# Performance work log

Hardware: AMD Instinct MI355X
Metric: run time of the kernel (lower is better)

## Reference

```python
import jax, jax.numpy as jnp
import numpy as np

N = 100_000      # num nodes
E = 6_400_000    # num edges
P = 12           # periods
F = 32           # output_size (TGCN hidden)


def setup_inputs() -> dict:
    key = jax.random.key(0)
    ks = jax.random.split(key, 16)
    g = lambda i, shape, s=0.1: jax.random.normal(ks[i], shape, dtype=jnp.float32) * s
    zf = jnp.zeros((F,), jnp.float32)
    return {
        "x": jax.random.normal(ks[0], (N, P), dtype=jnp.float32),
        "edge_index": jax.random.randint(ks[1], (2, E), 0, N, dtype=jnp.int64),
        "edge_weight": jax.random.uniform(ks[2], (E,), dtype=jnp.float32),
        "attention": g(3, (P,), 1.0),            # A3TGCN learned period attention
        # GCNConv weights: in_channels=1 -> weight is effectively a length-F vector
        "wc_z": g(4, (F,)), "bc_z": zf,
        "wc_r": g(5, (F,)), "bc_r": zf,
        "wc_h": g(6, (F,)), "bc_h": zf,
        # TGCN gate linears: Linear(2F, F) with bias
        "wl_z": g(7, (2 * F, F)), "bl_z": zf,
        "wl_r": g(8, (2 * F, F)), "bl_r": zf,
        "wl_h": g(9, (2 * F, F)), "bl_h": zf,
        # final Linear(F, 1)
        "w_out": g(10, (F, 1)), "b_out": jnp.zeros((1,), jnp.float32),
    }


def reference(x, edge_index, edge_weight, attention,
              wc_z, bc_z, wc_r, bc_r, wc_h, bc_h,
              wl_z, bl_z, wl_r, bl_r, wl_h, bl_h,
              w_out, b_out):
    n = x.shape[0]
    src, dst = edge_index[0], edge_index[1]

    # GCN normalization with added self-loops (weight 1): D^{-1/2} (A + I) D^{-1/2}
    deg = jax.ops.segment_sum(edge_weight, dst, num_segments=n) + 1.0
    dinv = jax.lax.rsqrt(deg)
    norm = dinv[src] * edge_weight * dinv[dst]          # (E,)

    # GCNConv is linear and in_channels == 1, so conv_g(X_p)_i = agg(X_p)_i * W_g + b_g
    # where agg is the normalized (self-loop augmented) scalar aggregation.
    # Aggregate all periods at once: (E, P) messages -> (N, P)
    agg = jax.ops.segment_sum(norm[:, None] * x[src], dst, num_segments=n)
    agg = agg + (dinv * dinv)[:, None] * x              # self-loop term, (N, P)

    probs = jax.nn.softmax(attention)                   # (P,)
    H0 = jnp.zeros((n, F), x.dtype)                     # A3TGCN calls TGCN with H=None each period
    H_acc = jnp.zeros((n, F), x.dtype)
    for p in range(P):                                  # small fixed structural loop
        s = agg[:, p, None]                             # (N, 1)
        conv_z = s * wc_z + bc_z                        # (N, F)
        conv_r = s * wc_r + bc_r
        conv_h = s * wc_h + bc_h
        Z = jax.nn.sigmoid(jnp.concatenate([conv_z, H0], axis=1) @ wl_z + bl_z)
        R = jax.nn.sigmoid(jnp.concatenate([conv_r, H0], axis=1) @ wl_r + bl_r)
        Ht = jnp.tanh(jnp.concatenate([conv_h, H0 * R], axis=1) @ wl_h + bl_h)
        Hp = Z * H0 + (1.0 - Z) * Ht                    # TGCN single step from zero state
        H_acc = H_acc + probs[p] * Hp

    h = jax.nn.relu(H_acc)
    return h @ w_out + b_out                            # (N, 1)
```

## Files before the change

kernel.cpp:

```cpp
#include <hip/hip_runtime.h>

#define NN 100000
#define EE 6400000
#define PP 12
#define FF 32

#define VV   128
#define BB   782
#define CAP  8832
#define K1B  800
#define CHK  8000
#define NBIN 784
#define AST  13
#define XST  16
#define NR   18

__global__ void precompute_k(const float* __restrict__ att,
                             const float* __restrict__ wc_z, const float* __restrict__ bc_z,
                             const float* __restrict__ wc_h, const float* __restrict__ bc_h,
                             const float* __restrict__ wl_z, const float* __restrict__ bl_z,
                             const float* __restrict__ wl_h, const float* __restrict__ bl_h,
                             float* __restrict__ tabs) {
    int j = threadIdx.x;
    if (j < FF) {
        float az = 0.f, cz = 0.f, ah = 0.f, ch = 0.f;
        for (int f = 0; f < FF; ++f) {
            float wz = wl_z[f * FF + j];
            float wh = wl_h[f * FF + j];
            az += wc_z[f] * wz;
            cz += bc_z[f] * wz;
            ah += wc_h[f] * wh;
            ch += bc_h[f] * wh;
        }
        tabs[16 + j]          = az;
        tabs[16 + FF + j]     = cz + bl_z[j];
        tabs[16 + 2 * FF + j] = ah;
        tabs[16 + 3 * FF + j] = ch + bl_h[j];
    } else if (j == FF) {
        float a[PP];
        float m = -1e30f;
        for (int p = 0; p < PP; ++p) { a[p] = att[p]; m = fmaxf(m, a[p]); }
        float s = 0.f;
        for (int p = 0; p < PP; ++p) { a[p] = __expf(a[p] - m); s += a[p]; }
        for (int p = 0; p < PP; ++p) tabs[p] = a[p] / s;
    }
}

__global__ __launch_bounds__(512) void bucketsort_k(const int* __restrict__ src,
                                                    const int* __restrict__ dst,
                                                    const float* __restrict__ ew,
                                                    uint2* __restrict__ recs,
                                                    unsigned short* __restrict__ T16) {
    __shared__ unsigned int perm[CHK];
    __shared__ int hist[NBIN];
    __shared__ int offs[NBIN];
    int tid = threadIdx.x;
    int blk = blockIdx.x;
    int beg = blk * CHK;

    for (int b = tid; b < NBIN; b += 512) hist[b] = 0;
    __syncthreads();

    for (int e = tid; e < CHK; e += 512)
        atomicAdd(&hist[dst[beg + e] >> 7], 1);
    __syncthreads();

    int i2   = 512 + tid;
    int own0 = hist[tid];
    int own1 = (i2 < NBIN) ? hist[i2] : 0;
    for (int off = 1; off < NBIN; off <<= 1) {
        int a0 = (tid >= off) ? hist[tid - off] : 0;
        int a1 = (i2 < NBIN) ? hist[i2 - off] : 0;
        __syncthreads();
        hist[tid] += a0;
        if (i2 < NBIN) hist[i2] += a1;
        __syncthreads();
    }
    offs[tid] = hist[tid] - own0;
    if (i2 < NBIN) offs[i2] = hist[i2] - own1;
    __syncthreads();

    for (int b = tid; b < BB + 1; b += 512)
        T16[(size_t)b * K1B + blk] = (unsigned short)offs[b];
    __syncthreads();

    for (int e = tid; e < CHK; e += 512) {
        int d = dst[beg + e];
        int p = atomicAdd(&offs[d >> 7], 1);
        perm[p] = ((unsigned)(d & (VV - 1)) << 13) | (unsigned)e;
    }
    __syncthreads();

    uint2* o = recs + (size_t)blk * CHK;
    for (int k = tid; k < CHK; k += 512) {
        unsigned pe = perm[k];
        int e = (int)(pe & 0x1FFFu);
        uint2 r;
        r.x = ((pe >> 13) << 17) | (unsigned)src[beg + e];
        r.y = __float_as_uint(ew[beg + e]);
        o[k] = r;
    }
}

__global__ __launch_bounds__(512) void deg2_k(const uint2* __restrict__ recs,
                                              const unsigned short* __restrict__ T16,
                                              const float* __restrict__ x,
                                              float* __restrict__ xds) {
    __shared__ unsigned long long wsum[VV];
    __shared__ int rstart[K1B];
    __shared__ int rpre[K1B + 1];
    int b = blockIdx.x;
    int tid = threadIdx.x;
    int i1 = tid + 512;

    if (tid < VV) wsum[tid] = 0ull;
    for (int k = tid; k < K1B; k += 512) {
        int s = T16[(size_t)b * K1B + k];
        int e = T16[(size_t)(b + 1) * K1B + k];
        rstart[k] = s;
        rpre[k]   = e - s;
    }
    __syncthreads();

    for (int off = 1; off < K1B; off <<= 1) {
        int a0 = (tid >= off) ? rpre[tid - off] : 0;
        int a1 = (i1 < K1B) ? rpre[i1 - off] : 0;
        __syncthreads();
        rpre[tid] += a0;
        if (i1 < K1B) rpre[i1] += a1;
        __syncthreads();
    }
    int inc0 = rpre[tid];
    int inc1 = (i1 < K1B) ? rpre[i1] : 0;
    __syncthreads();
    if (tid == 0) rpre[0] = 0;
    rpre[tid + 1] = inc0;
    if (i1 < K1B) rpre[i1 + 1] = inc1;
    __syncthreads();

    int n = rpre[K1B];
    for (int k = tid; k < n; k += 512) {
        int r = 0;
        #pragma unroll
        for (int s = 512; s; s >>= 1) {
            int c = r + s;
            if (c < K1B && rpre[c] <= k) r = c;
        }
        uint2 v = recs[(size_t)r * CHK + rstart[r] + (k - rpre[r])];
        unsigned long long w = (unsigned long long)(__uint_as_float(v.y) * 4294967296.0f);
        atomicAdd(&wsum[v.x >> 17], w);
    }
    __syncthreads();

    int node = b * VV + tid;
    if (tid < VV && node < NN) {
        float wf = (float)wsum[tid] * (1.0f / 4294967296.0f);
        float dv = rsqrtf(wf + 1.0f);
        const float4* xr = (const float4*)(x + (size_t)node * PP);
        float4* xo = (float4*)(xds + ((size_t)node << 4));
        #pragma unroll
        for (int q = 0; q < 3; ++q) {
            float4 v = xr[q];
            v.x *= dv; v.y *= dv; v.z *= dv; v.w *= dv;
            xo[q] = v;
        }
        xds[((size_t)node << 4) + 12] = dv;
    }
}

__global__ __launch_bounds__(512) void sortagg_k(const uint2* __restrict__ recs,
                                                 const unsigned short* __restrict__ T16,
                                                 const float* __restrict__ xds,
                                                 const float* __restrict__ tabs,
                                                 const float* __restrict__ w_out,
                                                 const float* __restrict__ b_out,
                                                 float* __restrict__ out) {
    __shared__ uint2 srec[CAP];
    __shared__ int   h[VV], starts_s[VV], offs[VV], cnts_s[VV];
    __shared__ int   rstart[K1B];
    __shared__ int   rpre[K1B + 1];
    int b = blockIdx.x;
    int tid = threadIdx.x;
    int i1 = tid + 512;

    if (tid < VV) h[tid] = 0;
    for (int k = tid; k < K1B; k += 512) {
        int s = T16[(size_t)b * K1B + k];
        int e = T16[(size_t)(b + 1) * K1B + k];
        rstart[k] = s;
        rpre[k]   = e - s;
    }
    __syncthreads();

    for (int off = 1; off < K1B; off <<= 1) {
        int a0 = (tid >= off) ? rpre[tid - off] : 0;
        int a1 = (i1 < K1B) ? rpre[i1 - off] : 0;
        __syncthreads();
        rpre[tid] += a0;
        if (i1 < K1B) rpre[i1] += a1;
        __syncthreads();
    }
    int inc0 = rpre[tid];
    int inc1 = (i1 < K1B) ? rpre[i1] : 0;
    __syncthreads();
    if (tid == 0) rpre[0] = 0;
    rpre[tid + 1] = inc0;
    if (i1 < K1B) rpre[i1 + 1] = inc1;
    __syncthreads();

    int n = min(rpre[K1B], 512 * NR);

    uint2 regs[NR];
    #pragma unroll
    for (int w = 0; w < NR; ++w) {
        int k = tid + w * 512;
        if (k < n) {
            int r = 0;
            #pragma unroll
            for (int s = 512; s; s >>= 1) {
                int c = r + s;
                if (c < K1B && rpre[c] <= k) r = c;
            }
            uint2 v = recs[(size_t)r * CHK + rstart[r] + (k - rpre[r])];
            regs[w] = v;
            atomicAdd(&h[v.x >> 17], 1);
        }
    }
    __syncthreads();

    int own = (tid < VV) ? h[tid] : 0;
    #pragma unroll
    for (int off = 1; off < VV; off <<= 1) {
        int t = (tid < VV && tid >= off) ? h[tid - off] : 0;
        __syncthreads();
        if (tid < VV) h[tid] += t;
        __syncthreads();
    }
    if (tid < VV) {
        int pre = h[tid] - own;
        starts_s[tid] = pre;
        offs[tid]     = pre;
        cnts_s[tid]   = own;
    }
    __syncthreads();

    #pragma unroll
    for (int w = 0; w < NR; ++w) {
        int k = tid + w * 512;
        if (k < n) {
            uint2 v = regs[w];
            int p = atomicAdd(&offs[v.x >> 17], 1);
            if (p < CAP) srec[p] = v;
        }
    }
    __syncthreads();

    float acc[PP];
    {
        int local = tid >> 2;
        int q     = tid & 3;
        int st = min(starts_s[local], CAP);
        int en = min(starts_s[local] + cnts_s[local], CAP);
        int cn = en - st;

        #pragma unroll
        for (int p = 0; p < PP; ++p) acc[p] = 0.f;

        for (int m = q; m < cn; m += 4) {
            uint2 v = srec[st + m];
            float c = __uint_as_float(v.y);
            const float4* xs = (const float4*)(xds + ((size_t)(v.x & 0x1FFFFu) << 4));
            float4 v0 = xs[0], v1 = xs[1], v2 = xs[2];
            acc[0] += c * v0.x;  acc[1] += c * v0.y;  acc[2]  += c * v0.z;  acc[3]  += c * v0.w;
            acc[4] += c * v1.x;  acc[5] += c * v1.y;  acc[6]  += c * v1.z;  acc[7]  += c * v1.w;
            acc[8] += c * v2.x;  acc[9] += c * v2.y;  acc[10] += c * v2.z;  acc[11] += c * v2.w;
        }

        #pragma unroll
        for (int p = 0; p < PP; ++p) {
            acc[p] += __shfl_xor(acc[p], 1, 4);
            acc[p] += __shfl_xor(acc[p], 2, 4);
        }
    }
    __syncthreads();

    float* agg = (float*)srec;
    if ((tid & 3) == 0) {
        float* ap = &agg[(tid >> 2) * AST];
        #pragma unroll
        for (int p = 0; p < PP; ++p) ap[p] = acc[p];
    }
    __syncthreads();

    int g = tid >> 5;
    int j = tid & 31;
    float azj = tabs[16 + j];
    float czj = tabs[16 + FF + j];
    float ahj = tabs[16 + 2 * FF + j];
    float chj = tabs[16 + 3 * FF + j];

    for (int nl = g; nl < VV; nl += 16) {
        int i = b * VV + nl;
        if (i >= NN) continue;
        float dv = xds[((size_t)i << 4) + 12];
        const float* ai = &agg[nl * AST];

        float accum = 0.f;
        #pragma unroll
        for (int p = 0; p < PP; ++p) {
            float sp = dv * (ai[p] + xds[((size_t)i << 4) + p]);
            float pr = tabs[p];
            float uz = sp * azj + czj;
            float uh = sp * ahj + chj;
            float one_minus_z = 1.0f / (1.0f + __expf(uz));
            float e2h = __expf(2.0f * uh);
            float th  = 1.0f - 2.0f / (e2h + 1.0f);
            accum += pr * one_minus_z * th;
        }
        float hv = fmaxf(accum, 0.f) * w_out[j];
        #pragma unroll
        for (int off = 16; off > 0; off >>= 1)
            hv += __shfl_xor(hv, off, 32);
        if (j == 0) out[i] = hv + b_out[0];
    }
}

__global__ __launch_bounds__(256) void deg_k(const int* __restrict__ dst,
                                             const float* __restrict__ ew,
                                             float* __restrict__ deg) {
    int stride = gridDim.x * blockDim.x;
    for (int e = blockIdx.x * blockDim.x + threadIdx.x; e < EE; e += stride)
        atomicAdd(&deg[dst[e]], ew[e]);
}

__global__ __launch_bounds__(256) void dinv_self_k(const float* __restrict__ x,
                                                   float* __restrict__ deg,
                                                   float* __restrict__ agg) {
    int i = blockIdx.x * blockDim.x + threadIdx.x;
    if (i >= NN) return;
    float d  = deg[i] + 1.0f;
    float dv = rsqrtf(d);
    deg[i]   = dv;
    float dv2 = dv * dv;
    const float4* xr = (const float4*)(x + (size_t)i * PP);
    float4* ar = (float4*)(agg + (size_t)i * PP);
    #pragma unroll
    for (int q = 0; q < 3; ++q) {
        float4 v = xr[q];
        v.x *= dv2; v.y *= dv2; v.z *= dv2; v.w *= dv2;
        ar[q] = v;
    }
}

__global__ __launch_bounds__(256) void agg_k(const int* __restrict__ src,
                                             const int* __restrict__ dst,
                                             const float* __restrict__ ew,
                                             const float* __restrict__ x,
                                             const float* __restrict__ dinv,
                                             float* __restrict__ agg) {
    int stride = gridDim.x * blockDim.x;
    for (int e = blockIdx.x * blockDim.x + threadIdx.x; e < EE; e += stride) {
        int s = src[e];
        int d = dst[e];
        float nw = dinv[s] * ew[e] * dinv[d];
        const float4* xs = (const float4*)(x + (size_t)s * PP);
        float* ad = agg + (size_t)d * PP;
        float4 v0 = xs[0], v1 = xs[1], v2 = xs[2];
        atomicAdd(&ad[0],  nw * v0.x);
        atomicAdd(&ad[1],  nw * v0.y);
        atomicAdd(&ad[2],  nw * v0.z);
        atomicAdd(&ad[3],  nw * v0.w);
        atomicAdd(&ad[4],  nw * v1.x);
        atomicAdd(&ad[5],  nw * v1.y);
        atomicAdd(&ad[6],  nw * v1.z);
        atomicAdd(&ad[7],  nw * v1.w);
        atomicAdd(&ad[8],  nw * v2.x);
        atomicAdd(&ad[9],  nw * v2.y);
        atomicAdd(&ad[10], nw * v2.z);
        atomicAdd(&ad[11], nw * v2.w);
    }
}

__global__ __launch_bounds__(256) void node_k(const float* __restrict__ agg,
                                              const float* __restrict__ tabs,
                                              const float* __restrict__ w_out,
                                              const float* __restrict__ b_out,
                                              float* __restrict__ out) {
    int t = blockIdx.x * blockDim.x + threadIdx.x;
    int i = t >> 5;
    int j = t & 31;
    if (i >= NN) return;
    float azj = tabs[16 + j];
    float czj = tabs[16 + FF + j];
    float ahj = tabs[16 + 2 * FF + j];
    float chj = tabs[16 + 3 * FF + j];
    float acc = 0.f;
    #pragma unroll
    for (int p = 0; p < PP; ++p) {
        float s  = agg[i * PP + p];
        float pr = tabs[p];
        float uz = s * azj + czj;
        float uh = s * ahj + chj;
        float one_minus_z = 1.0f / (1.0f + __expf(uz));
        float e2h = __expf(2.0f * uh);
        float th  = 1.0f - 2.0f / (e2h + 1.0f);
        acc += pr * one_minus_z * th;
    }
    float h = fmaxf(acc, 0.f) * w_out[j];
    #pragma unroll
    for (int off = 16; off > 0; off >>= 1)
        h += __shfl_xor(h, off, 32);
    if (j == 0) out[i] = h + b_out[0];
}

extern "C" void kernel_launch(void* const* d_in, const int* in_sizes, int n_in,
                              void* d_out, int out_size, void* d_ws, size_t ws_size,
                              hipStream_t stream) {
    const float* x    = (const float*)d_in[0];
    const int*   ei   = (const int*)d_in[1];
    const float* ew   = (const float*)d_in[2];
    const float* att  = (const float*)d_in[3];
    const float* wc_z = (const float*)d_in[4];
    const float* bc_z = (const float*)d_in[5];
    const float* wc_h = (const float*)d_in[8];
    const float* bc_h = (const float*)d_in[9];
    const float* wl_z = (const float*)d_in[10];
    const float* bl_z = (const float*)d_in[11];
    const float* wl_h = (const float*)d_in[14];
    const float* bl_h = (const float*)d_in[15];
    const float* wout = (const float*)d_in[16];
    const float* bout = (const float*)d_in[17];
    float* out = (float*)d_out;

    const int* src = ei;
    const int* dst = ei + EE;

    size_t region = (size_t)EE * sizeof(uint2);
    size_t tbl_sz = (size_t)783 * K1B * sizeof(unsigned short);
    size_t xds_sz = (size_t)NN * XST * sizeof(float);
    size_t need   = region + tbl_sz + xds_sz + 4096;

    if (ws_size >= need) {
        uint2*          recs = (uint2*)d_ws;
        unsigned short* T16  = (unsigned short*)((char*)d_ws + region);
        float*          xds  = (float*)((char*)d_ws + region + tbl_sz);
        float*          tabs = (float*)((char*)d_ws + region + tbl_sz + xds_sz);

        precompute_k<<<1, 64, 0, stream>>>(att, wc_z, bc_z, wc_h, bc_h, wl_z, bl_z, wl_h, bl_h, tabs);
        bucketsort_k<<<K1B, 512, 0, stream>>>(src, dst, ew, recs, T16);
        deg2_k<<<BB, 512, 0, stream>>>(recs, T16, x, xds);
        sortagg_k<<<BB, 512, 0, stream>>>(recs, T16, xds, tabs, wout, bout, out);
    } else {
        float* deg  = (float*)d_ws;
        float* agg  = deg + NN;
        float* tabs = agg + (size_t)NN * PP;

        hipMemsetAsync(deg, 0, NN * sizeof(float), stream);
        precompute_k<<<1, 64, 0, stream>>>(att, wc_z, bc_z, wc_h, bc_h, wl_z, bl_z, wl_h, bl_h, tabs);
        deg_k<<<4096, 256, 0, stream>>>(dst, ew, deg);
        dinv_self_k<<<(NN + 255) / 256, 256, 0, stream>>>(x, deg, agg);
        agg_k<<<8192, 256, 0, stream>>>(src, dst, ew, x, deg, agg);
        node_k<<<NN * 32 / 256, 256, 0, stream>>>(agg, tabs, wout, bout, out);
    }
}
```

Before: 357.0 us.

## Split per-bucket degree and aggregation work across two segment blocks

The degree and aggregation kernels now launch two blocks per 128-node bucket, each handling half of the 800 sort chunks. Partial degree sums and partial aggregates go to global buffers, and new xds_k and epi_k kernels combine them. The intent is to raise parallelism and occupancy by halving shared memory and register records per block (CAP2, NR2). The cost is two extra kernel launches and extra global traffic for the partial results.

```diff
diff --git a/kernel.cpp b/kernel.cpp
--- a/kernel.cpp
+++ b/kernel.cpp
@@ -5,15 +5,16 @@
 #define PP 12
 #define FF 32
 
-#define VV   128
-#define BB   782
-#define CAP  8832
-#define K1B  800
-#define CHK  8000
-#define NBIN 784
-#define AST  13
-#define XST  16
-#define NR   18
+#define VV    128
+#define BB    782
+#define K1B   800
+#define CHK   8000
+#define NBIN  784
+#define XST   16
+#define K1SEG 400
+#define CAP2  4576
+#define NR2   9
+#define FPSI  (1.0f / 4294967296.0f)
 
 __global__ void precompute_k(const float* __restrict__ att,
                              const float* __restrict__ wc_z, const float* __restrict__ bc_z,
@@ -104,124 +105,121 @@
 
 __global__ __launch_bounds__(512) void deg2_k(const uint2* __restrict__ recs,
                                               const unsigned short* __restrict__ T16,
-                                              const float* __restrict__ x,
-                                              float* __restrict__ xds) {
+                                              unsigned long long* __restrict__ pdeg) {
     __shared__ unsigned long long wsum[VV];
-    __shared__ int rstart[K1B];
-    __shared__ int rpre[K1B + 1];
-    int b = blockIdx.x;
+    __shared__ unsigned short rstart[K1SEG];
+    __shared__ int rpre[K1SEG + 1];
+    int b   = blockIdx.x >> 1;
+    int seg = blockIdx.x & 1;
     int tid = threadIdx.x;
-    int i1 = tid + 512;
+    int k0  = seg * K1SEG;
 
     if (tid < VV) wsum[tid] = 0ull;
-    for (int k = tid; k < K1B; k += 512) {
-        int s = T16[(size_t)b * K1B + k];
-        int e = T16[(size_t)(b + 1) * K1B + k];
-        rstart[k] = s;
-        rpre[k]   = e - s;
-    }
-    __syncthreads();
-
-    for (int off = 1; off < K1B; off <<= 1) {
-        int a0 = (tid >= off) ? rpre[tid - off] : 0;
-        int a1 = (i1 < K1B) ? rpre[i1 - off] : 0;
-        __syncthreads();
-        rpre[tid] += a0;
-        if (i1 < K1B) rpre[i1] += a1;
-        __syncthreads();
-    }
-    int inc0 = rpre[tid];
-    int inc1 = (i1 < K1B) ? rpre[i1] : 0;
+    if (tid < K1SEG) {
+        int s = T16[(size_t)b * K1B + k0 + tid];
+        int e = T16[(size_t)(b + 1) * K1B + k0 + tid];
+        rstart[tid] = (unsigned short)s;
+        rpre[tid]   = e - s;
+    }
+    __syncthreads();
+
+    for (int off = 1; off < K1SEG; off <<= 1) {
+        int a = (tid < K1SEG && tid >= off) ? rpre[tid - off] : 0;
+        __syncthreads();
+        if (tid < K1SEG) rpre[tid] += a;
+        __syncthreads();
+    }
+    int inc = (tid < K1SEG) ? rpre[tid] : 0;
     __syncthreads();
     if (tid == 0) rpre[0] = 0;
-    rpre[tid + 1] = inc0;
-    if (i1 < K1B) rpre[i1 + 1] = inc1;
-    __syncthreads();
-
-    int n = rpre[K1B];
+    if (tid < K1SEG) rpre[tid + 1] = inc;
+    __syncthreads();
+
+    int n = rpre[K1SEG];
     for (int k = tid; k < n; k += 512) {
         int r = 0;
         #pragma unroll
-        for (int s = 512; s; s >>= 1) {
+        for (int s = 256; s; s >>= 1) {
             int c = r + s;
-            if (c < K1B && rpre[c] <= k) r = c;
+            if (c < K1SEG && rpre[c] <= k) r = c;
         }
-        uint2 v = recs[(size_t)r * CHK + rstart[r] + (k - rpre[r])];
+        uint2 v = recs[(size_t)(k0 + r) * CHK + rstart[r] + (k - rpre[r])];
         unsigned long long w = (unsigned long long)(__uint_as_float(v.y) * 4294967296.0f);
         atomicAdd(&wsum[v.x >> 17], w);
     }
     __syncthreads();
 
     int node = b * VV + tid;
-    if (tid < VV && node < NN) {
-        float wf = (float)wsum[tid] * (1.0f / 4294967296.0f);
-        float dv = rsqrtf(wf + 1.0f);
-        const float4* xr = (const float4*)(x + (size_t)node * PP);
-        float4* xo = (float4*)(xds + ((size_t)node << 4));
-        #pragma unroll
-        for (int q = 0; q < 3; ++q) {
-            float4 v = xr[q];
-            v.x *= dv; v.y *= dv; v.z *= dv; v.w *= dv;
-            xo[q] = v;
-        }
-        xds[((size_t)node << 4) + 12] = dv;
-    }
+    if (tid < VV && node < NN)
+        pdeg[(size_t)seg * NN + node] = wsum[tid];
+}
+
+__global__ __launch_bounds__(256) void xds_k(const unsigned long long* __restrict__ pdeg,
+                                             const float* __restrict__ x,
+                                             float* __restrict__ xds) {
+    int i = blockIdx.x * 256 + threadIdx.x;
+    if (i >= NN) return;
+    float wf = (float)(pdeg[i] + pdeg[(size_t)NN + i]) * FPSI;
+    float dv = rsqrtf(wf + 1.0f);
+    const float4* xr = (const float4*)(x + (size_t)i * PP);
+    float4* xo = (float4*)(xds + ((size_t)i << 4));
+    #pragma unroll
+    for (int q = 0; q < 3; ++q) {
+        float4 v = xr[q];
+        v.x *= dv; v.y *= dv; v.z *= dv; v.w *= dv;
+        xo[q] = v;
+    }
+    xds[((size_t)i << 4) + 12] = dv;
 }
 
 __global__ __launch_bounds__(512) void sortagg_k(const uint2* __restrict__ recs,
                                                  const unsigned short* __restrict__ T16,
                                                  const float* __restrict__ xds,
-                                                 const float* __restrict__ tabs,
-                                                 const float* __restrict__ w_out,
-                                                 const float* __restrict__ b_out,
-                                                 float* __restrict__ out) {
-    __shared__ uint2 srec[CAP];
-    __shared__ int   h[VV], starts_s[VV], offs[VV], cnts_s[VV];
-    __shared__ int   rstart[K1B];
-    __shared__ int   rpre[K1B + 1];
-    int b = blockIdx.x;
+                                                 float* __restrict__ pagg) {
+    __shared__ uint2 srec[CAP2];
+    __shared__ int   h[VV], starts_s[VV], offs[VV];
+    __shared__ unsigned short rstart[K1SEG];
+    __shared__ int   rpre[K1SEG + 1];
+    int b   = blockIdx.x >> 1;
+    int seg = blockIdx.x & 1;
     int tid = threadIdx.x;
-    int i1 = tid + 512;
+    int k0  = seg * K1SEG;
 
     if (tid < VV) h[tid] = 0;
-    for (int k = tid; k < K1B; k += 512) {
-        int s = T16[(size_t)b * K1B + k];
-        int e = T16[(size_t)(b + 1) * K1B + k];
-        rstart[k] = s;
-        rpre[k]   = e - s;
-    }
-    __syncthreads();
-
-    for (int off = 1; off < K1B; off <<= 1) {
-        int a0 = (tid >= off) ? rpre[tid - off] : 0;
-        int a1 = (i1 < K1B) ? rpre[i1 - off] : 0;
-        __syncthreads();
-        rpre[tid] += a0;
-        if (i1 < K1B) rpre[i1] += a1;
-        __syncthreads();
-    }
-    int inc0 = rpre[tid];
-    int inc1 = (i1 < K1B) ? rpre[i1] : 0;
+    if (tid < K1SEG) {
+        int s = T16[(size_t)b * K1B + k0 + tid];
+        int e = T16[(size_t)(b + 1) * K1B + k0 + tid];
+        rstart[tid] = (unsigned short)s;
+        rpre[tid]   = e - s;
+    }
+    __syncthreads();
+
+    for (int off = 1; off < K1SEG; off <<= 1) {
+        int a = (tid < K1SEG && tid >= off) ? rpre[tid - off] : 0;
+        __syncthreads();
+        if (tid < K1SEG) rpre[tid] += a;
+        __syncthreads();
+    }
+    int inc = (tid < K1SEG) ? rpre[tid] : 0;
     __syncthreads();
     if (tid == 0) rpre[0] = 0;
-    rpre[tid + 1] = inc0;
-    if (i1 < K1B) rpre[i1 + 1] = inc1;
-    __syncthreads();
-
-    int n = min(rpre[K1B], 512 * NR);
-
-    uint2 regs[NR];
-    #pragma unroll
-    for (int w = 0; w < NR; ++w) {
+    if (tid < K1SEG) rpre[tid + 1] = inc;
+    __syncthreads();
+
+    int n = min(rpre[K1SEG], 512 * NR2);
+
+    uint2 regs[NR2];
+    #pragma unroll
+    for (int w = 0; w < NR2; ++w) {
         int k = tid + w * 512;
         if (k < n) {
             int r = 0;
             #pragma unroll
-            for (int s = 512; s; s >>= 1) {
+            for (int s = 256; s; s >>= 1) {
                 int c = r + s;
-                if (c < K1B && rpre[c] <= k) r = c;
+                if (c < K1SEG && rpre[c] <= k) r = c;
             }
-            uint2 v = recs[(size_t)r * CHK + rstart[r] + (k - rpre[r])];
+            uint2 v = recs[(size_t)(k0 + r) * CHK + rstart[r] + (k - rpre[r])];
             regs[w] = v;
             atomicAdd(&h[v.x >> 17], 1);
         }
@@ -240,58 +238,59 @@
         int pre = h[tid] - own;
         starts_s[tid] = pre;
         offs[tid]     = pre;
-        cnts_s[tid]   = own;
-    }
-    __syncthreads();
-
-    #pragma unroll
-    for (int w = 0; w < NR; ++w) {
+    }
+    __syncthreads();
+
+    #pragma unroll
+    for (int w = 0; w < NR2; ++w) {
         int k = tid + w * 512;
         if (k < n) {
             uint2 v = regs[w];
             int p = atomicAdd(&offs[v.x >> 17], 1);
-            if (p < CAP) srec[p] = v;
+            if (p < CAP2) srec[p] = v;
         }
     }
     __syncthreads();
 
+    int local = tid >> 2;
+    int q     = tid & 3;
+    int st = min(starts_s[local], CAP2);
+    int en = min(h[local], CAP2);
+
     float acc[PP];
-    {
-        int local = tid >> 2;
-        int q     = tid & 3;
-        int st = min(starts_s[local], CAP);
-        int en = min(starts_s[local] + cnts_s[local], CAP);
-        int cn = en - st;
-
-        #pragma unroll
-        for (int p = 0; p < PP; ++p) acc[p] = 0.f;
-
-        for (int m = q; m < cn; m += 4) {
-            uint2 v = srec[st + m];
-            float c = __uint_as_float(v.y);
-            const float4* xs = (const float4*)(xds + ((size_t)(v.x & 0x1FFFFu) << 4));
-            float4 v0 = xs[0], v1 = xs[1], v2 = xs[2];
-            acc[0] += c * v0.x;  acc[1] += c * v0.y;  acc[2]  += c * v0.z;  acc[3]  += c * v0.w;
-            acc[4] += c * v1.x;  acc[5] += c * v1.y;  acc[6]  += c * v1.z;  acc[7]  += c * v1.w;
-            acc[8] += c * v2.x;  acc[9] += c * v2.y;  acc[10] += c * v2.z;  acc[11] += c * v2.w;
-        }
-
-        #pragma unroll
-        for (int p = 0; p < PP; ++p) {
-            acc[p] += __shfl_xor(acc[p], 1, 4);
-            acc[p] += __shfl_xor(acc[p], 2, 4);
-        }
-    }
-    __syncthreads();
-
-    float* agg = (float*)srec;
-    if ((tid & 3) == 0) {
-        float* ap = &agg[(tid >> 2) * AST];
-        #pragma unroll
-        for (int p = 0; p < PP; ++p) ap[p] = acc[p];
-    }
-    __syncthreads();
-
+    #pragma unroll
+    for (int p = 0; p < PP; ++p) acc[p] = 0.f;
+
+    for (int m = st + q; m < en; m += 4) {
+        uint2 v = srec[m];
+        float c = __uint_as_float(v.y);
+        const float4* xs = (const float4*)(xds + ((size_t)(v.x & 0x1FFFFu) << 4));
+        float4 v0 = xs[0], v1 = xs[1], v2 = xs[2];
+        acc[0] += c * v0.x;  acc[1] += c * v0.y;  acc[2]  += c * v0.z;  acc[3]  += c * v0.w;
+        acc[4] += c * v1.x;  acc[5] += c * v1.y;  acc[6]  += c * v1.z;  acc[7]  += c * v1.w;
+        acc[8] += c * v2.x;  acc[9] += c * v2.y;  acc[10] += c * v2.z;  acc[11] += c * v2.w;
+    }
+
+    #pragma unroll
+    for (int p = 0; p < PP; ++p) {
+        acc[p] += __shfl_xor(acc[p], 1, 4);
+        acc[p] += __shfl_xor(acc[p], 2, 4);
+    }
+
+    float* ap = pagg + ((size_t)(seg * BB + b) * VV + local) * PP;
+    ap[3 * q + 0] = acc[3 * q + 0];
+    ap[3 * q + 1] = acc[3 * q + 1];
+    ap[3 * q + 2] = acc[3 * q + 2];
+}
+
+__global__ __launch_bounds__(512) void epi_k(const float* __restrict__ pagg,
+                                             const float* __restrict__ xds,
+                                             const float* __restrict__ tabs,
+                                             const float* __restrict__ w_out,
+                                             const float* __restrict__ b_out,
+                                             float* __restrict__ out) {
+    int b = blockIdx.x;
+    int tid = threadIdx.x;
     int g = tid >> 5;
     int j = tid & 31;
     float azj = tabs[16 + j];
@@ -303,12 +302,14 @@
         int i = b * VV + nl;
         if (i >= NN) continue;
         float dv = xds[((size_t)i << 4) + 12];
-        const float* ai = &agg[nl * AST];
+        const float* a0 = pagg + ((size_t)b * VV + nl) * PP;
+        const float* a1 = pagg + ((size_t)(BB + b) * VV + nl) * PP;
 
         float accum = 0.f;
         #pragma unroll
         for (int p = 0; p < PP; ++p) {
-            float sp = dv * (ai[p] + xds[((size_t)i << 4) + p]);
+            float ai = a0[p] + a1[p];
+            float sp = dv * (ai + xds[((size_t)i << 4) + p]);
             float pr = tabs[p];
             float uz = sp * azj + czj;
             float uh = sp * ahj + chj;
@@ -435,21 +436,28 @@
     const int* src = ei;
     const int* dst = ei + EE;
 
-    size_t region = (size_t)EE * sizeof(uint2);
-    size_t tbl_sz = (size_t)783 * K1B * sizeof(unsigned short);
-    size_t xds_sz = (size_t)NN * XST * sizeof(float);
-    size_t need   = region + tbl_sz + xds_sz + 4096;
+    size_t region  = (size_t)EE * sizeof(uint2);
+    size_t tbl_sz  = (((size_t)(BB + 1) * K1B * 2) + 63) & ~63ull;
+    size_t xds_sz  = (size_t)NN * XST * sizeof(float);
+    size_t pdeg_sz = (size_t)2 * NN * sizeof(unsigned long long);
+    size_t pagg_sz = (size_t)2 * BB * VV * PP * sizeof(float);
+    size_t need    = region + tbl_sz + xds_sz + pdeg_sz + pagg_sz + 4096;
 
     if (ws_size >= need) {
-        uint2*          recs = (uint2*)d_ws;
-        unsigned short* T16  = (unsigned short*)((char*)d_ws + region);
-        float*          xds  = (float*)((char*)d_ws + region + tbl_sz);
-        float*          tabs = (float*)((char*)d_ws + region + tbl_sz + xds_sz);
+        char* base = (char*)d_ws;
+        uint2*              recs = (uint2*)base;                 base += region;
+        unsigned short*     T16  = (unsigned short*)base;        base += tbl_sz;
+        float*              xds  = (float*)base;                 base += xds_sz;
+        unsigned long long* pdeg = (unsigned long long*)base;    base += pdeg_sz;
+        float*              pagg = (float*)base;                 base += pagg_sz;
+        float*              tabs = (float*)base;
 
         precompute_k<<<1, 64, 0, stream>>>(att, wc_z, bc_z, wc_h, bc_h, wl_z, bl_z, wl_h, bl_h, tabs);
         bucketsort_k<<<K1B, 512, 0, stream>>>(src, dst, ew, recs, T16);
-        deg2_k<<<BB, 512, 0, stream>>>(recs, T16, x, xds);
-        sortagg_k<<<BB, 512, 0, stream>>>(recs, T16, xds, tabs, wout, bout, out);
+        deg2_k<<<BB * 2, 512, 0, stream>>>(recs, T16, pdeg);
+        xds_k<<<(NN + 255) / 256, 256, 0, stream>>>(pdeg, x, xds);
+        sortagg_k<<<BB * 2, 512, 0, stream>>>(recs, T16, xds, pagg);
+        epi_k<<<BB, 512, 0, stream>>>(pagg, xds, tabs, wout, bout, out);
     } else {
         float* deg  = (float*)d_ws;
         float* agg  = deg + NN;
```

Measured after the change: 362.0 us. No clear change (+1.4%).
